# Kernel tuning notes

Hardware: AMD Instinct MI355X
Metric: run time of the kernel (lower is better)

Reference implementation:

```python
import jax, jax.numpy as jnp
import numpy as np

B, IC, HC = 262144, 128, 128


def setup_inputs() -> dict:
    key = jax.random.key(0)
    ks = jax.random.split(key, 12)
    s_ih = 1.0 / np.sqrt(IC)
    s_hh = 1.0 / np.sqrt(HC)
    return {
        "x": jax.random.normal(ks[0], (B, IC), jnp.float32),
        "u": jax.random.uniform(ks[1], (B, 1), jnp.float32),
        "h": jax.random.normal(ks[2], (B, HC), jnp.float32) * 0.1,
        "c": jax.random.normal(ks[3], (B, HC), jnp.float32) * 0.1,
        "delta_u": jax.random.uniform(ks[4], (B, 1), jnp.float32),
        "skip": jax.random.randint(ks[5], (B,), 0, 2) == 1,
        # LSTMCell params (PyTorch gate order: i, f, g, o)
        "W_ih": jax.random.normal(ks[6], (4 * HC, IC), jnp.float32) * s_ih,
        "W_hh": jax.random.normal(ks[7], (4 * HC, HC), jnp.float32) * s_hh,
        "b_ih": jnp.zeros((4 * HC,), jnp.float32),
        "b_hh": jnp.zeros((4 * HC,), jnp.float32),
        # Linear(hc -> 1), bias initialized to 1 per the module
        "lin_w": jax.random.normal(ks[8], (1, HC), jnp.float32) * s_hh,
        "lin_b": jnp.ones((1,), jnp.float32),
    }


def _ste_round(u):
    # straight-through estimator: forward round, identity backward
    return u + jax.lax.stop_gradient(jnp.round(u) - u)


def reference(x, u, h, c, delta_u, skip, W_ih, W_hh, b_ih, b_hh, lin_w, lin_b):
    bu = _ste_round(u)  # [B,1]

    # --- no-skip branch: LSTM cell + update-gate linear ---
    gates = x @ W_ih.T + b_ih + h @ W_hh.T + b_hh  # [B,4*HC]
    i, f, g, o = jnp.split(gates, 4, axis=1)
    i = jax.nn.sigmoid(i)
    f = jax.nn.sigmoid(f)
    g = jnp.tanh(g)
    o = jax.nn.sigmoid(o)
    nc = f * c + i * g
    nh = o * jnp.tanh(nc)
    new_h_n = nh * bu
    new_c_n = nc * bu
    delta_u_n = jax.nn.sigmoid(new_c_n @ lin_w.T + lin_b)  # [B,1]
    new_u_n = delta_u_n * bu

    # --- skip branch: decay state, accumulate u ---
    keep = 1.0 - bu
    new_h_s = h * keep
    new_c_s = c * keep
    new_u_s = jnp.clip(u + delta_u, 0.0, 1.0) * keep

    # --- recombine by skip mask (equivalent to the gather/scatter routing) ---
    sk = skip[:, None]
    new_u = jnp.where(sk, new_u_s, new_u_n)
    new_h = jnp.where(sk, new_h_s, new_h_n)
    new_c = jnp.where(sk, new_c_s, new_c_n)
    d_u = jnp.where(sk, delta_u, delta_u_n)

    n_skips_after = jnp.ceil(0.5 / new_u) - 1.0
    return new_u, (new_h, new_c), d_u, n_skips_after
```

## Files before the change

### kernel.cpp

```cpp
#include <hip/hip_runtime.h>


typedef _Float16 half8  __attribute__((ext_vector_type(8)));
typedef _Float16 half4v __attribute__((ext_vector_type(4)));
typedef float    float4v __attribute__((ext_vector_type(4)));

#define B_ROWS 262144
#define TM 64
#define XPITCH 264
#define XPLANE (TM * XPITCH)
#define WCOMP  131072

__device__ __forceinline__ float sigmoidf_(float v) { return 1.0f / (1.0f + __expf(-v)); }
__device__ __forceinline__ float tanhf_(float v) {
    float ax = fabsf(v);
    float t = __expf(-2.0f * ax);
    float r = (1.0f - t) / (1.0f + t);
    return copysignf(r, v);
}

__global__ void prep_kernel(const float* __restrict__ W_ih, const float* __restrict__ W_hh,
                            const float* __restrict__ b_ih, const float* __restrict__ b_hh,
                            _Float16* __restrict__ Wp, float* __restrict__ bias) {
    int idx = blockIdx.x * 256 + threadIdx.x;
    int n = idx >> 8, k = idx & 255;
    float v = (k < 128) ? W_ih[n * 128 + k] : W_hh[n * 128 + (k - 128)];
    _Float16 wh = (_Float16)v;
    _Float16 wl = (_Float16)(v - (float)wh);
    int kb = k >> 5, quad = (k >> 3) & 3, j = k & 7;
    int nt = n >> 4, n16 = n & 15, lane = quad * 16 + n16;
    int base = (kb * 32 + nt) * 512 + lane * 8 + j;
    Wp[base] = wh;
    Wp[WCOMP + base] = wl;
    if (idx < 512) bias[idx] = b_ih[idx] + b_hh[idx];
}

__launch_bounds__(256, 2)
__global__ void lstm_kernel(const float* __restrict__ x, const float* __restrict__ u,
                            const float* __restrict__ h, const float* __restrict__ c,
                            const float* __restrict__ delta_u, const int* __restrict__ skip,
                            const float* __restrict__ lin_w, const float* __restrict__ lin_b,
                            const _Float16* __restrict__ Wp, const float* __restrict__ bias,
                            float* __restrict__ out) {
    __shared__ __align__(16) _Float16 Xs[2 * XPLANE];
    __shared__ float zw[4][TM];
    __shared__ float s_u[TM], s_du[TM];
    __shared__ int   s_sk[TM];

    const int tid = threadIdx.x;
    const int m0  = blockIdx.x * TM;

    #pragma unroll
    for (int i = 0; i < 16; ++i) {
        int idx = i * 256 + tid;
        int r = idx >> 6, c4 = (idx & 63) * 4;
        float4v v;
        if (c4 < 128) v = *(const float4v*)&x[(size_t)(m0 + r) * 128 + c4];
        else          v = *(const float4v*)&h[(size_t)(m0 + r) * 128 + (c4 - 128)];
        half4v hi, lo;
        #pragma unroll
        for (int e = 0; e < 4; ++e) {
            _Float16 hh = (_Float16)v[e];
            hi[e] = hh;
            lo[e] = (_Float16)(v[e] - (float)hh);
        }
        *(half4v*)&Xs[r * XPITCH + c4]          = hi;
        *(half4v*)&Xs[XPLANE + r * XPITCH + c4] = lo;
    }
    if (tid < TM) {
        s_u[tid]  = u[m0 + tid];
        s_du[tid] = delta_u[m0 + tid];
        s_sk[tid] = skip[m0 + tid];
    }
    __syncthreads();

    const int lane = tid & 63, w = tid >> 6;
    const int n16 = lane & 15, quad = lane >> 4;

    int ntid[8];
    #pragma unroll
    for (int g = 0; g < 4; ++g)
        #pragma unroll
        for (int p = 0; p < 2; ++p) ntid[g * 2 + p] = w * 2 + g * 8 + p;

    float4v acc[8][4];
    #pragma unroll
    for (int t = 0; t < 8; ++t)
        #pragma unroll
        for (int mt = 0; mt < 4; ++mt) acc[t][mt] = (float4v){0.f, 0.f, 0.f, 0.f};

    #pragma unroll 1
    for (int kb = 0; kb < 8; ++kb) {
        half8 bh[8], bl[8];
        #pragma unroll
        for (int t = 0; t < 8; ++t) {
            const _Float16* bp = Wp + (size_t)(kb * 32 + ntid[t]) * 512 + lane * 8;
            bh[t] = *(const half8*)bp;
            bl[t] = *(const half8*)(bp + WCOMP);
        }
        half8 ah[4], al[4];
        const int koff = kb * 32 + quad * 8;
        #pragma unroll
        for (int mt = 0; mt < 4; ++mt) {
            int m = mt * 16 + n16;
            ah[mt] = *(const half8*)&Xs[m * XPITCH + koff];
            al[mt] = *(const half8*)&Xs[XPLANE + m * XPITCH + koff];
        }
        #pragma unroll
        for (int t = 0; t < 8; ++t)
            #pragma unroll
            for (int mt = 0; mt < 4; ++mt) {
                acc[t][mt] = __builtin_amdgcn_mfma_f32_16x16x32_f16(ah[mt], bh[t], acc[t][mt], 0, 0, 0);
                acc[t][mt] = __builtin_amdgcn_mfma_f32_16x16x32_f16(al[mt], bh[t], acc[t][mt], 0, 0, 0);
                acc[t][mt] = __builtin_amdgcn_mfma_f32_16x16x32_f16(ah[mt], bl[t], acc[t][mt], 0, 0, 0);
            }
    }

    float* out_u  = out;
    float* out_h  = out + (size_t)B_ROWS;
    float* out_c  = out + (size_t)B_ROWS * 129;
    float* out_du = out + (size_t)B_ROWS * 257;
    float* out_ns = out + (size_t)B_ROWS * 258;

    float zpart[4][4];
    #pragma unroll
    for (int mt = 0; mt < 4; ++mt)
        #pragma unroll
        for (int reg = 0; reg < 4; ++reg) zpart[mt][reg] = 0.f;

    #pragma unroll
    for (int p = 0; p < 2; ++p) {
        int hc = w * 32 + p * 16 + n16;
        float bi = bias[hc], bf = bias[hc + 128], bg = bias[hc + 256], bo = bias[hc + 384];
        float lw = lin_w[hc];
        #pragma unroll
        for (int mt = 0; mt < 4; ++mt) {
            #pragma unroll
            for (int reg = 0; reg < 4; ++reg) {
                int row = mt * 16 + quad * 4 + reg;
                size_t m = (size_t)(m0 + row);
                float iv = sigmoidf_(acc[0 * 2 + p][mt][reg] + bi);
                float fv = sigmoidf_(acc[1 * 2 + p][mt][reg] + bf);
                float gv = tanhf_  (acc[2 * 2 + p][mt][reg] + bg);
                float ov = sigmoidf_(acc[3 * 2 + p][mt][reg] + bo);
                float cin = c[m * 128 + hc];
                float ncv = fv * cin + iv * gv;
                float nhv = ov * tanhf_(ncv);
                float buv = rintf(s_u[row]);
                float keep = 1.0f - buv;
                bool  sk = s_sk[row] != 0;
                float hin = (float)Xs[row * XPITCH + 128 + hc]
                          + (float)Xs[XPLANE + row * XPITCH + 128 + hc];
                out_h[m * 128 + hc] = sk ? hin * keep : nhv * buv;
                out_c[m * 128 + hc] = sk ? cin * keep : ncv * buv;
                zpart[mt][reg] += ncv * lw;
            }
        }
    }

    #pragma unroll
    for (int mt = 0; mt < 4; ++mt)
        #pragma unroll
        for (int reg = 0; reg < 4; ++reg) {
            float v = zpart[mt][reg];
            v += __shfl_xor(v, 1, 64);
            v += __shfl_xor(v, 2, 64);
            v += __shfl_xor(v, 4, 64);
            v += __shfl_xor(v, 8, 64);
            if (n16 == 0) zw[w][mt * 16 + quad * 4 + reg] = v;
        }
    __syncthreads();

    if (tid < TM) {
        int row = tid;
        float z = zw[0][row] + zw[1][row] + zw[2][row] + zw[3][row];
        float buv = rintf(s_u[row]);
        float keep = 1.0f - buv;
        bool  sk = s_sk[row] != 0;
        float dun = sigmoidf_(z * buv + lin_b[0]);
        float nu = sk ? fminf(fmaxf(s_u[row] + s_du[row], 0.0f), 1.0f) * keep
                      : dun * buv;
        float duo = sk ? s_du[row] : dun;
        float nsk = ceilf(0.5f / nu) - 1.0f;
        if (!__builtin_isfinite(nsk)) nsk = 1.0e30f;
        size_t m = (size_t)(m0 + row);
        out_u[m]  = nu;
        out_du[m] = duo;
        out_ns[m] = nsk;
    }
}

extern "C" void kernel_launch(void* const* d_in, const int* in_sizes, int n_in,
                              void* d_out, int out_size, void* d_ws, size_t ws_size,
                              hipStream_t stream) {
    const float* x     = (const float*)d_in[0];
    const float* u     = (const float*)d_in[1];
    const float* h     = (const float*)d_in[2];
    const float* c     = (const float*)d_in[3];
    const float* du    = (const float*)d_in[4];
    const int*   skip  = (const int*)d_in[5];
    const float* W_ih  = (const float*)d_in[6];
    const float* W_hh  = (const float*)d_in[7];
    const float* b_ih  = (const float*)d_in[8];
    const float* b_hh  = (const float*)d_in[9];
    const float* lin_w = (const float*)d_in[10];
    const float* lin_b = (const float*)d_in[11];
    float* outp = (float*)d_out;
    _Float16* Wp = (_Float16*)d_ws;
    float* bias  = (float*)((char*)d_ws + 2 * WCOMP * sizeof(_Float16));

    prep_kernel<<<512, 256, 0, stream>>>(W_ih, W_hh, b_ih, b_hh, Wp, bias);
    lstm_kernel<<<B_ROWS / TM, 256, 0, stream>>>(x, u, h, c, du, skip, lin_w, lin_b,
                                                 Wp, bias, outp);
}
```

Baseline: 751.8 us.

## Compact active rows and run LSTM GEMM only on non-skipped, unrounded-zero rows

Adds a classify kernel that writes outputs directly for skipped or bu==0 rows and compacts the indices of active rows (skip==0 and round(u)==1) through an atomic counter. The GEMM kernel then gathers only those rows, computing gates and the update gate for a fraction of the batch, and blocks past the active count exit early. This avoids MFMA work and x/h reads for rows whose outputs do not depend on the LSTM cell. The cost is an extra kernel launch, an atomic, gathered (non-contiguous) row loads, and output order for active rows that depends on atomic scheduling.

New measurement: 616.5 us. 1.22x faster.

```diff
diff --git a/kernel.cpp b/kernel.cpp
--- a/kernel.cpp
+++ b/kernel.cpp
@@ -21,7 +21,9 @@
 
 __global__ void prep_kernel(const float* __restrict__ W_ih, const float* __restrict__ W_hh,
                             const float* __restrict__ b_ih, const float* __restrict__ b_hh,
-                            _Float16* __restrict__ Wp, float* __restrict__ bias) {
+                            _Float16* __restrict__ Wp, float* __restrict__ bias,
+                            int* __restrict__ counter) {
+    if (blockIdx.x == 0 && threadIdx.x == 0) *counter = 0;
     int idx = blockIdx.x * 256 + threadIdx.x;
     int n = idx >> 8, k = idx & 255;
     float v = (k < 128) ? W_ih[n * 128 + k] : W_hh[n * 128 + (k - 128)];
@@ -35,28 +37,104 @@
     if (idx < 512) bias[idx] = b_ih[idx] + b_hh[idx];
 }
 
+__global__ void classify_kernel(const float* __restrict__ u, const float* __restrict__ h,
+                                const float* __restrict__ c, const float* __restrict__ delta_u,
+                                const int* __restrict__ skip, const float* __restrict__ lin_b,
+                                int* __restrict__ counter, int* __restrict__ act_idx,
+                                float* __restrict__ out) {
+    __shared__ int s_cat[TM];
+    const int tid = threadIdx.x;
+    const int m0  = blockIdx.x * TM;
+
+    float* out_u  = out;
+    float* out_h  = out + (size_t)B_ROWS;
+    float* out_c  = out + (size_t)B_ROWS * 129;
+    float* out_du = out + (size_t)B_ROWS * 257;
+    float* out_ns = out + (size_t)B_ROWS * 258;
+
+    if (tid < TM) {
+        int row = m0 + tid;
+        float uv  = u[row];
+        float duv = delta_u[row];
+        int   sk  = skip[row];
+        float buv = rintf(uv);
+        bool active = (sk == 0) && (buv != 0.0f);
+        s_cat[tid] = active ? 2 : ((sk != 0 && buv == 0.0f) ? 1 : 0);
+
+        if (!active) {
+            float nu, duo;
+            if (sk != 0) {
+                nu  = (buv == 0.0f) ? fminf(fmaxf(uv + duv, 0.0f), 1.0f) : 0.0f;
+                duo = duv;
+            } else {
+                nu  = 0.0f;
+                duo = sigmoidf_(lin_b[0]);
+            }
+            float nsk = ceilf(0.5f / nu) - 1.0f;
+            if (!__builtin_isfinite(nsk)) nsk = 1.0e30f;
+            out_u[row]  = nu;
+            out_du[row] = duo;
+            out_ns[row] = nsk;
+        }
+        unsigned long long mask = __ballot(active);
+        int nact = __popcll(mask);
+        int base = 0;
+        if (tid == 0 && nact) base = atomicAdd(counter, nact);
+        base = __shfl(base, 0, 64);
+        if (active) {
+            int pos = __popcll(mask & ((1ull << tid) - 1ull));
+            act_idx[base + pos] = row;
+        }
+    }
+    __syncthreads();
+
+    #pragma unroll
+    for (int it = 0; it < 8; ++it) {
+        int r = it * 8 + (tid >> 5);
+        int cat = s_cat[r];
+        if (cat == 2) continue;
+        size_t m = (size_t)(m0 + r);
+        int c4 = (tid & 31) * 4;
+        float4v vh = {0.f, 0.f, 0.f, 0.f}, vc = {0.f, 0.f, 0.f, 0.f};
+        if (cat == 1) {
+            vh = *(const float4v*)&h[m * 128 + c4];
+            vc = *(const float4v*)&c[m * 128 + c4];
+        }
+        *(float4v*)&out_h[m * 128 + c4] = vh;
+        *(float4v*)&out_c[m * 128 + c4] = vc;
+    }
+}
+
 __launch_bounds__(256, 2)
-__global__ void lstm_kernel(const float* __restrict__ x, const float* __restrict__ u,
-                            const float* __restrict__ h, const float* __restrict__ c,
-                            const float* __restrict__ delta_u, const int* __restrict__ skip,
+__global__ void gemm_kernel(const float* __restrict__ x, const float* __restrict__ h,
+                            const float* __restrict__ c,
                             const float* __restrict__ lin_w, const float* __restrict__ lin_b,
                             const _Float16* __restrict__ Wp, const float* __restrict__ bias,
+                            const int* __restrict__ counter, const int* __restrict__ act_idx,
                             float* __restrict__ out) {
+    const int n_act = *counter;
+    if ((int)blockIdx.x * TM >= n_act) return;
+
     __shared__ __align__(16) _Float16 Xs[2 * XPLANE];
     __shared__ float zw[4][TM];
-    __shared__ float s_u[TM], s_du[TM];
-    __shared__ int   s_sk[TM];
+    __shared__ int   s_rid[TM];
 
     const int tid = threadIdx.x;
-    const int m0  = blockIdx.x * TM;
+
+    if (tid < TM) {
+        int g = blockIdx.x * TM + tid;
+        s_rid[tid] = act_idx[g < n_act ? g : n_act - 1];
+    }
+    __syncthreads();
 
     #pragma unroll
     for (int i = 0; i < 16; ++i) {
-        int idx = i * 256 + tid;
-        int r = idx >> 6, c4 = (idx & 63) * 4;
+        int id2 = i * 256 + tid;
+        int r = id2 >> 6, c4 = (id2 & 63) * 4;
+        size_t srow = (size_t)s_rid[r];
         float4v v;
-        if (c4 < 128) v = *(const float4v*)&x[(size_t)(m0 + r) * 128 + c4];
-        else          v = *(const float4v*)&h[(size_t)(m0 + r) * 128 + (c4 - 128)];
+        if (c4 < 128) v = *(const float4v*)&x[srow * 128 + c4];
+        else          v = *(const float4v*)&h[srow * 128 + (c4 - 128)];
         half4v hi, lo;
         #pragma unroll
         for (int e = 0; e < 4; ++e) {
@@ -66,11 +144,6 @@
         }
         *(half4v*)&Xs[r * XPITCH + c4]          = hi;
         *(half4v*)&Xs[XPLANE + r * XPITCH + c4] = lo;
-    }
-    if (tid < TM) {
-        s_u[tid]  = u[m0 + tid];
-        s_du[tid] = delta_u[m0 + tid];
-        s_sk[tid] = skip[m0 + tid];
     }
     __syncthreads();
 
@@ -138,7 +211,8 @@
             #pragma unroll
             for (int reg = 0; reg < 4; ++reg) {
                 int row = mt * 16 + quad * 4 + reg;
-                size_t m = (size_t)(m0 + row);
+                bool valid = blockIdx.x * TM + row < n_act;
+                size_t m = (size_t)s_rid[row];
                 float iv = sigmoidf_(acc[0 * 2 + p][mt][reg] + bi);
                 float fv = sigmoidf_(acc[1 * 2 + p][mt][reg] + bf);
                 float gv = tanhf_  (acc[2 * 2 + p][mt][reg] + bg);
@@ -146,13 +220,10 @@
                 float cin = c[m * 128 + hc];
                 float ncv = fv * cin + iv * gv;
                 float nhv = ov * tanhf_(ncv);
-                float buv = rintf(s_u[row]);
-                float keep = 1.0f - buv;
-                bool  sk = s_sk[row] != 0;
-                float hin = (float)Xs[row * XPITCH + 128 + hc]
-                          + (float)Xs[XPLANE + row * XPITCH + 128 + hc];
-                out_h[m * 128 + hc] = sk ? hin * keep : nhv * buv;
-                out_c[m * 128 + hc] = sk ? cin * keep : ncv * buv;
+                if (valid) {
+                    out_h[m * 128 + hc] = nhv;
+                    out_c[m * 128 + hc] = ncv;
+                }
                 zpart[mt][reg] += ncv * lw;
             }
         }
@@ -173,20 +244,16 @@
 
     if (tid < TM) {
         int row = tid;
-        float z = zw[0][row] + zw[1][row] + zw[2][row] + zw[3][row];
-        float buv = rintf(s_u[row]);
-        float keep = 1.0f - buv;
-        bool  sk = s_sk[row] != 0;
-        float dun = sigmoidf_(z * buv + lin_b[0]);
-        float nu = sk ? fminf(fmaxf(s_u[row] + s_du[row], 0.0f), 1.0f) * keep
-                      : dun * buv;
-        float duo = sk ? s_du[row] : dun;
-        float nsk = ceilf(0.5f / nu) - 1.0f;
-        if (!__builtin_isfinite(nsk)) nsk = 1.0e30f;
-        size_t m = (size_t)(m0 + row);
-        out_u[m]  = nu;
-        out_du[m] = duo;
-        out_ns[m] = nsk;
+        if (blockIdx.x * TM + row < n_act) {
+            float z = zw[0][row] + zw[1][row] + zw[2][row] + zw[3][row];
+            float dun = sigmoidf_(z + lin_b[0]);
+            float nsk = ceilf(0.5f / dun) - 1.0f;
+            if (!__builtin_isfinite(nsk)) nsk = 1.0e30f;
+            size_t m = (size_t)s_rid[row];
+            out_u[m]  = dun;
+            out_du[m] = dun;
+            out_ns[m] = nsk;
+        }
     }
 }
 
@@ -206,10 +273,15 @@
     const float* lin_w = (const float*)d_in[10];
     const float* lin_b = (const float*)d_in[11];
     float* outp = (float*)d_out;
-    _Float16* Wp = (_Float16*)d_ws;
-    float* bias  = (float*)((char*)d_ws + 2 * WCOMP * sizeof(_Float16));
-
-    prep_kernel<<<512, 256, 0, stream>>>(W_ih, W_hh, b_ih, b_hh, Wp, bias);
-    lstm_kernel<<<B_ROWS / TM, 256, 0, stream>>>(x, u, h, c, du, skip, lin_w, lin_b,
-                                                 Wp, bias, outp);
-}
+
+    _Float16* Wp   = (_Float16*)d_ws;
+    float* bias    = (float*)((char*)d_ws + 2 * WCOMP * sizeof(_Float16));
+    int* counter   = (int*)((char*)d_ws + 2 * WCOMP * sizeof(_Float16) + 2048);
+    int* act_idx   = (int*)((char*)d_ws + 2 * WCOMP * sizeof(_Float16) + 2048 + 64);
+
+    prep_kernel<<<512, 256, 0, stream>>>(W_ih, W_hh, b_ih, b_hh, Wp, bias, counter);
+    classify_kernel<<<B_ROWS / TM, 256, 0, stream>>>(u, h, c, du, skip, lin_b,
+                                                     counter, act_idx, outp);
+    gemm_kernel<<<B_ROWS / TM, 256, 0, stream>>>(x, h, c, lin_w, lin_b, Wp, bias,
+                                                 counter, act_idx, outp);
+}
```
